# Kernel optimization log

Hardware: AMD Instinct MI355X
Metric: run time of the kernel (lower is better)

## Reference

```python
import jax, jax.numpy as jnp
import numpy as np


def _binomial_blur(k, C):
    a = np.array([1.0, 2.0, 1.0]) if k == 3 else np.ones(k)
    f = a[:, None] * a[None, :]
    f = f / f.sum()
    # HWIO depthwise kernel: (k, k, 1, C)
    return jnp.asarray(np.broadcast_to(f[:, :, None, None], (k, k, 1, C)).copy(), jnp.float32)


def setup_inputs() -> dict:
    key = jax.random.key(0)
    x = jax.random.normal(key, (32, 64, 64, 128), dtype=jnp.float32)
    blur_kernel = _binomial_blur(3, 128)  # fixed (non-learned) binomial low-pass filter
    return {"x": x, "blur_kernel": blur_kernel}


def reference(x, blur_kernel):
    B, T, F, C = x.shape
    # 1) 2x2 max pool, stride 1, SAME (pool_mode='max')
    p = jax.lax.reduce_window(x, -jnp.inf, jax.lax.max,
                              (1, 2, 2, 1), (1, 1, 1, 1), 'SAME')
    # 2) depthwise antialiasing blur, 3x3, SAME
    b = jax.lax.conv_general_dilated(
        p, blur_kernel, window_strides=(1, 1), padding='SAME',
        dimension_numbers=('NHWC', 'HWIO', 'NHWC'), feature_group_count=C)
    # 3) polyphase decomposition (stride 2). Order matches permute_polyphase:
    #    p0=(even,even), p1=(odd,even), p2=(even,odd), p3=(odd,odd)
    cands = jnp.stack([b[:, 0::2, 0::2], b[:, 1::2, 0::2],
                       b[:, 0::2, 1::2], b[:, 1::2, 1::2]], axis=1)  # [B,4,T/2,F/2,C]
    # 4) l2 criterion: pick candidate with max l2 norm per example
    norms = jnp.sqrt(jnp.sum(cands * cands, axis=(2, 3, 4)))  # [B,4]
    idx = jnp.argmax(norms, axis=1)  # [B]
    # 5) gather selected polyphase component
    out = jnp.take_along_axis(cands, idx[:, None, None, None, None], axis=1)[:, 0]
    return out  # [B, T/2, F/2, C]
```

## Files before the change

kernel.cpp:

```cpp
#include <hip/hip_runtime.h>
#include <hip/hip_bf16.h>
#include <float.h>


#define NEGF (-FLT_MAX)

__device__ __forceinline__ float4 f4max(float4 a, float4 b) {
    return make_float4(fmaxf(a.x, b.x), fmaxf(a.y, b.y),
                       fmaxf(a.z, b.z), fmaxf(a.w, b.w));
}
__device__ __forceinline__ float4 f4add(float4 a, float4 b) {
    return make_float4(a.x + b.x, a.y + b.y, a.z + b.z, a.w + b.w);
}
__device__ __forceinline__ float4 f4b3(float4 a, float4 b, float4 c) {
    return make_float4(fmaf(2.f, b.x, a.x + c.x), fmaf(2.f, b.y, a.y + c.y),
                       fmaf(2.f, b.z, a.z + c.z), fmaf(2.f, b.w, a.w + c.w));
}
__device__ __forceinline__ float4 Z4() { return make_float4(0.f, 0.f, 0.f, 0.f); }

__device__ __forceinline__ float bf2f(unsigned short h) {
    return __uint_as_float((unsigned)h << 16);
}
__device__ __forceinline__ ushort2 pk2(float a, float b) {
    __hip_bfloat162 h = __float22bfloat162_rn(make_float2(a, b));
    union { __hip_bfloat162 h2; ushort2 u2; } cv; cv.h2 = h;
    return cv.u2;
}
__device__ __forceinline__ ushort4 packbf(float4 v, float s) {
    ushort2 lo = pk2(v.x * s, v.y * s);
    ushort2 hi = pk2(v.z * s, v.w * s);
    ushort4 r; r.x = lo.x; r.y = lo.y; r.z = hi.x; r.w = hi.y;
    return r;
}

__device__ __forceinline__ void load_hm(const float4* __restrict__ xb, int r,
                                        const int voff[7], float4 hm[6]) {
    if (r < 0 || r > 63) {
#pragma unroll
        for (int j = 0; j < 6; ++j) hm[j] = make_float4(NEGF, NEGF, NEGF, NEGF);
        return;
    }
    const float4* row = xb + (size_t)r * (64 * 32);
    float4 xv[7];
#pragma unroll
    for (int j = 0; j < 7; ++j) xv[j] = row[voff[j]];
#pragma unroll
    for (int j = 0; j < 6; ++j) hm[j] = f4max(xv[j], xv[j + 1]);
}

__global__ __launch_bounds__(256, 2) void aps_norm_store_kernel(
        const float* __restrict__ xg, float4* __restrict__ partial4,
        ushort4* __restrict__ cand) {
    int blk = blockIdx.x;
    int h = blk & 7, ct = (blk >> 3) & 1, b = blk >> 4;
    int tid = threadIdx.x;
    int cg = tid & 31;
    int gc = ct * 8 + (tid >> 5);
    int C = gc * 4;
    int t0 = h * 8;

    const float4* xb = (const float4*)xg + (size_t)b * (64 * 64 * 32);

    int voff[7];
#pragma unroll
    for (int j = 0; j < 7; ++j) {
        int c = C - 1 + j;
        c = c < 0 ? 0 : (c > 63 ? 63 : c);
        voff[j] = c * 32 + cg;
    }
    bool zp0 = (gc == 0), zp5 = (gc == 15);

    float4 hmP[6];
    load_hm(xb, t0 - 1, voff, hmP);
    float4 xvA[7], xvB[7];
    {
        const float4* rowA = xb + (size_t)t0 * (64 * 32);
        const float4* rowB = xb + (size_t)(t0 + 1) * (64 * 32);
#pragma unroll
        for (int j = 0; j < 7; ++j) xvA[j] = rowA[voff[j]];
#pragma unroll
        for (int j = 0; j < 7; ++j) xvB[j] = rowB[voff[j]];
    }

    float4 uM1[4], uM2[4];
#pragma unroll
    for (int j = 0; j < 4; ++j) { uM1[j] = Z4(); uM2[j] = Z4(); }
    float aEE = 0.f, aEO = 0.f, aOE = 0.f, aOO = 0.f;

#pragma unroll
    for (int i = 0; i < 10; ++i) {
        int pr = t0 - 1 + i;
        int rN = pr + 3; rN = rN > 63 ? 63 : rN;
        const float4* rowN = xb + (size_t)rN * (64 * 32);
        float4 xvN[7];
#pragma unroll
        for (int j = 0; j < 7; ++j) xvN[j] = rowN[voff[j]];

        bool rv = (pr + 1) <= 63;
        float4 hmN[6];
#pragma unroll
        for (int j = 0; j < 6; ++j)
            hmN[j] = rv ? f4max(xvA[j], xvA[j + 1])
                        : make_float4(NEGF, NEGF, NEGF, NEGF);

        float4 p[6];
#pragma unroll
        for (int j = 0; j < 6; ++j) p[j] = f4max(hmP[j], hmN[j]);
        if (zp0) p[0] = Z4();
        if (zp5) p[5] = Z4();
        bool urow = (pr >= 0) & (pr <= 63);
        float4 u[4];
#pragma unroll
        for (int j = 0; j < 4; ++j)
            u[j] = urow ? f4b3(p[j], p[j + 1], p[j + 2]) : Z4();

        if (i >= 2) {
            float4 bb[4];
            float sE = 0.f, sO = 0.f;
#pragma unroll
            for (int j = 0; j < 4; ++j) {
                bb[j] = f4b3(uM2[j], uM1[j], u[j]);
                float d = bb[j].x * bb[j].x + bb[j].y * bb[j].y
                        + bb[j].z * bb[j].z + bb[j].w * bb[j].w;
                if (j & 1) sO += d; else sE += d;
            }
            sE *= (1.f / 256.f); sO *= (1.f / 256.f);
            if ((i & 1) == 0) { aEE += sE; aEO += sO; }
            else              { aOE += sE; aOO += sO; }

            int tp = i & 1;
            int tt = (t0 + i - 2) >> 1;
            size_t rowbase = (((size_t)b * 32 + tt) * 32) * 32 + cg;
            size_t f0 = rowbase + (size_t)(2 * gc) * 32;
            size_t f1 = rowbase + (size_t)(2 * gc + 1) * 32;
            size_t rT = (size_t)tp * 1048576;
            size_t rF = (size_t)(tp + 2) * 1048576;
            cand[rT + f0] = packbf(bb[0], 0.0625f);
            cand[rF + f0] = packbf(bb[1], 0.0625f);
            cand[rT + f1] = packbf(bb[2], 0.0625f);
            cand[rF + f1] = packbf(bb[3], 0.0625f);
        }

#pragma unroll
        for (int j = 0; j < 6; ++j) hmP[j] = hmN[j];
#pragma unroll
        for (int j = 0; j < 7; ++j) { xvA[j] = xvB[j]; xvB[j] = xvN[j]; }
#pragma unroll
        for (int j = 0; j < 4; ++j) { uM2[j] = uM1[j]; uM1[j] = u[j]; }
    }

    __shared__ float4 sm4[256];
    sm4[tid] = make_float4(aEE, aEO, aOE, aOO);
    __syncthreads();
    for (int s = 128; s >= 1; s >>= 1) {
        if (tid < s) sm4[tid] = f4add(sm4[tid], sm4[tid + s]);
        __syncthreads();
    }
    if (tid == 0) partial4[blk] = sm4[0];
}

__global__ __launch_bounds__(256) void aps_copy_kernel(
        const ushort4* __restrict__ cand, const float4* __restrict__ partial4,
        float4* __restrict__ outg) {
    __shared__ int ksm;
    int b = blockIdx.x >> 7;
    if (threadIdx.x == 0) {
        float4 tot = Z4();
        for (int j = 0; j < 16; ++j) tot = f4add(tot, partial4[b * 16 + j]);
        float n0 = tot.x, n1 = tot.z, n2 = tot.y, n3 = tot.w;
        int k = 0; float best = n0;
        if (n1 > best) { best = n1; k = 1; }
        if (n2 > best) { best = n2; k = 2; }
        if (n3 > best) { best = n3; k = 3; }
        ksm = k;
    }
    __syncthreads();
    int k = ksm;
    int gid = blockIdx.x * 256 + threadIdx.x;
    ushort4 v = cand[(size_t)k * 1048576 + gid];
    outg[gid] = make_float4(bf2f(v.x), bf2f(v.y), bf2f(v.z), bf2f(v.w));
}


__global__ __launch_bounds__(256, 2) void aps_norm_kernel(
        const float* __restrict__ xg, float4* __restrict__ partial4) {
    int blk = blockIdx.x;
    int h = blk & 7, ct = (blk >> 3) & 1, b = blk >> 4;
    int tid = threadIdx.x;
    int cg = tid & 31;
    int gc = ct * 8 + (tid >> 5);
    int C = gc * 4;
    int t0 = h * 8;

    const float4* xb = (const float4*)xg + (size_t)b * (64 * 64 * 32);

    int voff[7];
#pragma unroll
    for (int j = 0; j < 7; ++j) {
        int c = C - 1 + j;
        c = c < 0 ? 0 : (c > 63 ? 63 : c);
        voff[j] = c * 32 + cg;
    }
    bool zp0 = (gc == 0), zp5 = (gc == 15);

    float4 hmP[6];
    load_hm(xb, t0 - 1, voff, hmP);
    float4 uM1[4], uM2[4];
#pragma unroll
    for (int j = 0; j < 4; ++j) { uM1[j] = Z4(); uM2[j] = Z4(); }
    float aEE = 0.f, aEO = 0.f, aOE = 0.f, aOO = 0.f;

#pragma unroll
    for (int i = 0; i < 10; ++i) {
        int pr = t0 - 1 + i;
        float4 hmN[6];
        load_hm(xb, pr + 1, voff, hmN);
        float4 p[6];
#pragma unroll
        for (int j = 0; j < 6; ++j) p[j] = f4max(hmP[j], hmN[j]);
        if (zp0) p[0] = Z4();
        if (zp5) p[5] = Z4();
        bool urow = (pr >= 0) & (pr <= 63);
        float4 u[4];
#pragma unroll
        for (int j = 0; j < 4; ++j)
            u[j] = urow ? f4b3(p[j], p[j + 1], p[j + 2]) : Z4();
#pragma unroll
        for (int j = 0; j < 6; ++j) hmP[j] = hmN[j];
        if (i >= 2) {
            float sE = 0.f, sO = 0.f;
#pragma unroll
            for (int j = 0; j < 4; ++j) {
                float4 bb = f4b3(uM2[j], uM1[j], u[j]);
                float d = bb.x * bb.x + bb.y * bb.y + bb.z * bb.z + bb.w * bb.w;
                if (j & 1) sO += d; else sE += d;
            }
            sE *= (1.f / 256.f); sO *= (1.f / 256.f);
            if ((i & 1) == 0) { aEE += sE; aEO += sO; }
            else              { aOE += sE; aOO += sO; }
        }
#pragma unroll
        for (int j = 0; j < 4; ++j) { uM2[j] = uM1[j]; uM1[j] = u[j]; }
    }

    __shared__ float4 sm4[256];
    sm4[tid] = make_float4(aEE, aEO, aOE, aOO);
    __syncthreads();
    for (int s = 128; s >= 1; s >>= 1) {
        if (tid < s) sm4[tid] = f4add(sm4[tid], sm4[tid + s]);
        __syncthreads();
    }
    if (tid == 0) partial4[blk] = sm4[0];
}

__global__ __launch_bounds__(256, 2) void aps_gather_kernel(
        const float* __restrict__ xg, const float4* __restrict__ partial4,
        float* __restrict__ outg) {
    int blk = blockIdx.x;
    int h = blk & 7, ct = (blk >> 3) & 1, b = blk >> 4;
    int tid = threadIdx.x;
    int cg = tid & 31;
    int gc = ct * 8 + (tid >> 5);
    int C = gc * 4;

    float4 tot = Z4();
    for (int j = 0; j < 16; ++j) tot = f4add(tot, partial4[b * 16 + j]);
    float n0 = tot.x, n1 = tot.z, n2 = tot.y, n3 = tot.w;
    int k = 0; float best = n0;
    if (n1 > best) { best = n1; k = 1; }
    if (n2 > best) { best = n2; k = 2; }
    if (n3 > best) { best = n3; k = 3; }
    int tp = k & 1, fp = k >> 1;

    const float4* xb = (const float4*)xg + (size_t)b * (64 * 64 * 32);
    float4* ob = (float4*)outg + (size_t)b * (32 * 32 * 32);

    int voff[7];
#pragma unroll
    for (int j = 0; j < 7; ++j) {
        int c = C - 1 + j;
        c = c < 0 ? 0 : (c > 63 ? 63 : c);
        voff[j] = c * 32 + cg;
    }
    bool zp0 = (gc == 0), zp5 = (gc == 15);

    int sbase = h * 8 + tp;
    float4 hmP[6];
    load_hm(xb, sbase - 1, voff, hmP);
    float4 uM1[2], uM2[2];
#pragma unroll
    for (int j = 0; j < 2; ++j) { uM1[j] = Z4(); uM2[j] = Z4(); }

#pragma unroll
    for (int i = 0; i < 9; ++i) {
        int pr = sbase - 1 + i;
        float4 hmN[6];
        load_hm(xb, pr + 1, voff, hmN);
        float4 p[6];
#pragma unroll
        for (int j = 0; j < 6; ++j) p[j] = f4max(hmP[j], hmN[j]);
        if (zp0) p[0] = Z4();
        if (zp5) p[5] = Z4();
        bool urow = (pr >= 0) & (pr <= 63);
        float4 u[2];
        if (fp == 0) {
            u[0] = urow ? f4b3(p[0], p[1], p[2]) : Z4();
            u[1] = urow ? f4b3(p[2], p[3], p[4]) : Z4();
        } else {
            u[0] = urow ? f4b3(p[1], p[2], p[3]) : Z4();
            u[1] = urow ? f4b3(p[3], p[4], p[5]) : Z4();
        }
#pragma unroll
        for (int j = 0; j < 6; ++j) hmP[j] = hmN[j];
        if (i >= 2 && (i & 1) == 0) {
            int tt = 4 * h + (i >> 1) - 1;
#pragma unroll
            for (int jj = 0; jj < 2; ++jj) {
                float4 bb = f4b3(uM2[jj], uM1[jj], u[jj]);
                bb.x *= 0.0625f; bb.y *= 0.0625f; bb.z *= 0.0625f; bb.w *= 0.0625f;
                int ff = 2 * gc + jj;
                ob[((size_t)tt * 32 + ff) * 32 + cg] = bb;
            }
        }
#pragma unroll
        for (int j = 0; j < 2; ++j) { uM2[j] = uM1[j]; uM1[j] = u[j]; }
    }
}

extern "C" void kernel_launch(void* const* d_in, const int* in_sizes, int n_in,
                              void* d_out, int out_size, void* d_ws, size_t ws_size,
                              hipStream_t stream) {
    const float* x = (const float*)d_in[0];
    float4* partial4 = (float4*)d_ws;
    const size_t CAND_OFF = 8192;
    const size_t CAND_BYTES = (size_t)4 * 32 * 32 * 32 * 128 * 2;
    float* out = (float*)d_out;

    if (ws_size >= CAND_OFF + CAND_BYTES) {
        ushort4* cand = (ushort4*)((char*)d_ws + CAND_OFF);
        aps_norm_store_kernel<<<512, 256, 0, stream>>>(x, partial4, cand);
        aps_copy_kernel<<<4096, 256, 0, stream>>>(cand, partial4, (float4*)out);
    } else {
        aps_norm_kernel<<<512, 256, 0, stream>>>(x, partial4);
        aps_gather_kernel<<<512, 256, 0, stream>>>(x, partial4, out);
    }
}
```

Measured before the change: 31.72 us.

## Halve per-thread column tile in norm-store kernel, doubling grid and occupancy

New measurement: 43.47 us. 37.0% more time.

```diff
diff --git a/kernel.cpp b/kernel.cpp
--- a/kernel.cpp
+++ b/kernel.cpp
@@ -33,58 +33,53 @@
     return r;
 }
 
-__device__ __forceinline__ void load_hm(const float4* __restrict__ xb, int r,
-                                        const int voff[7], float4 hm[6]) {
-    if (r < 0 || r > 63) {
-#pragma unroll
-        for (int j = 0; j < 6; ++j) hm[j] = make_float4(NEGF, NEGF, NEGF, NEGF);
-        return;
-    }
-    const float4* row = xb + (size_t)r * (64 * 32);
-    float4 xv[7];
-#pragma unroll
-    for (int j = 0; j < 7; ++j) xv[j] = row[voff[j]];
-#pragma unroll
-    for (int j = 0; j < 6; ++j) hm[j] = f4max(xv[j], xv[j + 1]);
-}
-
-__global__ __launch_bounds__(256, 2) void aps_norm_store_kernel(
+__global__ __launch_bounds__(256, 4) void aps_norm_store_kernel(
         const float* __restrict__ xg, float4* __restrict__ partial4,
         ushort4* __restrict__ cand) {
     int blk = blockIdx.x;
-    int h = blk & 7, ct = (blk >> 3) & 1, b = blk >> 4;
+    int h = blk & 7, ct = (blk >> 3) & 3, b = blk >> 5;
     int tid = threadIdx.x;
     int cg = tid & 31;
-    int gc = ct * 8 + (tid >> 5);
-    int C = gc * 4;
+    int P = ct * 8 + (tid >> 5);
+    int C = P * 2;
     int t0 = h * 8;
 
     const float4* xb = (const float4*)xg + (size_t)b * (64 * 64 * 32);
 
-    int voff[7];
-#pragma unroll
-    for (int j = 0; j < 7; ++j) {
+    int voff[5];
+#pragma unroll
+    for (int j = 0; j < 5; ++j) {
         int c = C - 1 + j;
         c = c < 0 ? 0 : (c > 63 ? 63 : c);
         voff[j] = c * 32 + cg;
     }
-    bool zp0 = (gc == 0), zp5 = (gc == 15);
-
-    float4 hmP[6];
-    load_hm(xb, t0 - 1, voff, hmP);
-    float4 xvA[7], xvB[7];
+    bool zpL = (P == 0), zpR = (P == 31);
+
+    float4 hmP[4];
+    if (t0 - 1 < 0) {
+#pragma unroll
+        for (int j = 0; j < 4; ++j) hmP[j] = make_float4(NEGF, NEGF, NEGF, NEGF);
+    } else {
+        const float4* rowP = xb + (size_t)(t0 - 1) * (64 * 32);
+        float4 xv[5];
+#pragma unroll
+        for (int j = 0; j < 5; ++j) xv[j] = rowP[voff[j]];
+#pragma unroll
+        for (int j = 0; j < 4; ++j) hmP[j] = f4max(xv[j], xv[j + 1]);
+    }
+    float4 xvA[5], xvB[5];
     {
         const float4* rowA = xb + (size_t)t0 * (64 * 32);
         const float4* rowB = xb + (size_t)(t0 + 1) * (64 * 32);
 #pragma unroll
-        for (int j = 0; j < 7; ++j) xvA[j] = rowA[voff[j]];
-#pragma unroll
-        for (int j = 0; j < 7; ++j) xvB[j] = rowB[voff[j]];
-    }
-
-    float4 uM1[4], uM2[4];
-#pragma unroll
-    for (int j = 0; j < 4; ++j) { uM1[j] = Z4(); uM2[j] = Z4(); }
+        for (int j = 0; j < 5; ++j) xvA[j] = rowA[voff[j]];
+#pragma unroll
+        for (int j = 0; j < 5; ++j) xvB[j] = rowB[voff[j]];
+    }
+
+    float4 uM1[2], uM2[2];
+#pragma unroll
+    for (int j = 0; j < 2; ++j) { uM1[j] = Z4(); uM2[j] = Z4(); }
     float aEE = 0.f, aEO = 0.f, aOE = 0.f, aOO = 0.f;
 
 #pragma unroll
@@ -92,61 +87,49 @@
         int pr = t0 - 1 + i;
         int rN = pr + 3; rN = rN > 63 ? 63 : rN;
         const float4* rowN = xb + (size_t)rN * (64 * 32);
-        float4 xvN[7];
-#pragma unroll
-        for (int j = 0; j < 7; ++j) xvN[j] = rowN[voff[j]];
+        float4 xvN[5];
+#pragma unroll
+        for (int j = 0; j < 5; ++j) xvN[j] = rowN[voff[j]];
 
         bool rv = (pr + 1) <= 63;
-        float4 hmN[6];
-#pragma unroll
-        for (int j = 0; j < 6; ++j)
+        float4 hmN[4];
+#pragma unroll
+        for (int j = 0; j < 4; ++j)
             hmN[j] = rv ? f4max(xvA[j], xvA[j + 1])
                         : make_float4(NEGF, NEGF, NEGF, NEGF);
 
-        float4 p[6];
-#pragma unroll
-        for (int j = 0; j < 6; ++j) p[j] = f4max(hmP[j], hmN[j]);
-        if (zp0) p[0] = Z4();
-        if (zp5) p[5] = Z4();
+        float4 p[4];
+#pragma unroll
+        for (int j = 0; j < 4; ++j) p[j] = f4max(hmP[j], hmN[j]);
+        if (zpL) p[0] = Z4();
+        if (zpR) p[3] = Z4();
         bool urow = (pr >= 0) & (pr <= 63);
-        float4 u[4];
-#pragma unroll
-        for (int j = 0; j < 4; ++j)
-            u[j] = urow ? f4b3(p[j], p[j + 1], p[j + 2]) : Z4();
+        float4 u[2];
+        u[0] = urow ? f4b3(p[0], p[1], p[2]) : Z4();
+        u[1] = urow ? f4b3(p[1], p[2], p[3]) : Z4();
 
         if (i >= 2) {
-            float4 bb[4];
-            float sE = 0.f, sO = 0.f;
-#pragma unroll
-            for (int j = 0; j < 4; ++j) {
-                bb[j] = f4b3(uM2[j], uM1[j], u[j]);
-                float d = bb[j].x * bb[j].x + bb[j].y * bb[j].y
-                        + bb[j].z * bb[j].z + bb[j].w * bb[j].w;
-                if (j & 1) sO += d; else sE += d;
-            }
-            sE *= (1.f / 256.f); sO *= (1.f / 256.f);
-            if ((i & 1) == 0) { aEE += sE; aEO += sO; }
-            else              { aOE += sE; aOO += sO; }
+            float4 bb0 = f4b3(uM2[0], uM1[0], u[0]);
+            float4 bb1 = f4b3(uM2[1], uM1[1], u[1]);
+            float dE = bb0.x * bb0.x + bb0.y * bb0.y + bb0.z * bb0.z + bb0.w * bb0.w;
+            float dO = bb1.x * bb1.x + bb1.y * bb1.y + bb1.z * bb1.z + bb1.w * bb1.w;
+            dE *= (1.f / 256.f); dO *= (1.f / 256.f);
+            if ((i & 1) == 0) { aEE += dE; aEO += dO; }
+            else              { aOE += dE; aOO += dO; }
 
             int tp = i & 1;
             int tt = (t0 + i - 2) >> 1;
-            size_t rowbase = (((size_t)b * 32 + tt) * 32) * 32 + cg;
-            size_t f0 = rowbase + (size_t)(2 * gc) * 32;
-            size_t f1 = rowbase + (size_t)(2 * gc + 1) * 32;
-            size_t rT = (size_t)tp * 1048576;
-            size_t rF = (size_t)(tp + 2) * 1048576;
-            cand[rT + f0] = packbf(bb[0], 0.0625f);
-            cand[rF + f0] = packbf(bb[1], 0.0625f);
-            cand[rT + f1] = packbf(bb[2], 0.0625f);
-            cand[rF + f1] = packbf(bb[3], 0.0625f);
+            size_t foff = (((size_t)b * 32 + tt) * 32 + P) * 32 + cg;
+            cand[(size_t)tp * 1048576 + foff]       = packbf(bb0, 0.0625f);
+            cand[(size_t)(tp + 2) * 1048576 + foff] = packbf(bb1, 0.0625f);
         }
 
 #pragma unroll
-        for (int j = 0; j < 6; ++j) hmP[j] = hmN[j];
-#pragma unroll
-        for (int j = 0; j < 7; ++j) { xvA[j] = xvB[j]; xvB[j] = xvN[j]; }
-#pragma unroll
-        for (int j = 0; j < 4; ++j) { uM2[j] = uM1[j]; uM1[j] = u[j]; }
+        for (int j = 0; j < 4; ++j) hmP[j] = hmN[j];
+#pragma unroll
+        for (int j = 0; j < 5; ++j) { xvA[j] = xvB[j]; xvB[j] = xvN[j]; }
+#pragma unroll
+        for (int j = 0; j < 2; ++j) { uM2[j] = uM1[j]; uM1[j] = u[j]; }
     }
 
     __shared__ float4 sm4[256];
@@ -166,7 +149,7 @@
     int b = blockIdx.x >> 7;
     if (threadIdx.x == 0) {
         float4 tot = Z4();
-        for (int j = 0; j < 16; ++j) tot = f4add(tot, partial4[b * 16 + j]);
+        for (int j = 0; j < 32; ++j) tot = f4add(tot, partial4[b * 32 + j]);
         float n0 = tot.x, n1 = tot.z, n2 = tot.y, n3 = tot.w;
         int k = 0; float best = n0;
         if (n1 > best) { best = n1; k = 1; }
@@ -181,6 +164,21 @@
     outg[gid] = make_float4(bf2f(v.x), bf2f(v.y), bf2f(v.z), bf2f(v.w));
 }
 
+
+__device__ __forceinline__ void load_hm7(const float4* __restrict__ xb, int r,
+                                         const int voff[7], float4 hm[6]) {
+    if (r < 0 || r > 63) {
+#pragma unroll
+        for (int j = 0; j < 6; ++j) hm[j] = make_float4(NEGF, NEGF, NEGF, NEGF);
+        return;
+    }
+    const float4* row = xb + (size_t)r * (64 * 32);
+    float4 xv[7];
+#pragma unroll
+    for (int j = 0; j < 7; ++j) xv[j] = row[voff[j]];
+#pragma unroll
+    for (int j = 0; j < 6; ++j) hm[j] = f4max(xv[j], xv[j + 1]);
+}
 
 __global__ __launch_bounds__(256, 2) void aps_norm_kernel(
         const float* __restrict__ xg, float4* __restrict__ partial4) {
@@ -204,7 +202,7 @@
     bool zp0 = (gc == 0), zp5 = (gc == 15);
 
     float4 hmP[6];
-    load_hm(xb, t0 - 1, voff, hmP);
+    load_hm7(xb, t0 - 1, voff, hmP);
     float4 uM1[4], uM2[4];
 #pragma unroll
     for (int j = 0; j < 4; ++j) { uM1[j] = Z4(); uM2[j] = Z4(); }
@@ -214,7 +212,7 @@
     for (int i = 0; i < 10; ++i) {
         int pr = t0 - 1 + i;
         float4 hmN[6];
-        load_hm(xb, pr + 1, voff, hmN);
+        load_hm7(xb, pr + 1, voff, hmN);
         float4 p[6];
 #pragma unroll
         for (int j = 0; j < 6; ++j) p[j] = f4max(hmP[j], hmN[j]);
@@ -286,7 +284,7 @@
 
     int sbase = h * 8 + tp;
     float4 hmP[6];
-    load_hm(xb, sbase - 1, voff, hmP);
+    load_hm7(xb, sbase - 1, voff, hmP);
     float4 uM1[2], uM2[2];
 #pragma unroll
     for (int j = 0; j < 2; ++j) { uM1[j] = Z4(); uM2[j] = Z4(); }
@@ -295,7 +293,7 @@
     for (int i = 0; i < 9; ++i) {
         int pr = sbase - 1 + i;
         float4 hmN[6];
-        load_hm(xb, pr + 1, voff, hmN);
+        load_hm7(xb, pr + 1, voff, hmN);
         float4 p[6];
 #pragma unroll
         for (int j = 0; j < 6; ++j) p[j] = f4max(hmP[j], hmN[j]);
@@ -332,13 +330,13 @@
                               hipStream_t stream) {
     const float* x = (const float*)d_in[0];
     float4* partial4 = (float4*)d_ws;
-    const size_t CAND_OFF = 8192;
+    const size_t CAND_OFF = 16384;
     const size_t CAND_BYTES = (size_t)4 * 32 * 32 * 32 * 128 * 2;
     float* out = (float*)d_out;
 
     if (ws_size >= CAND_OFF + CAND_BYTES) {
         ushort4* cand = (ushort4*)((char*)d_ws + CAND_OFF);
-        aps_norm_store_kernel<<<512, 256, 0, stream>>>(x, partial4, cand);
+        aps_norm_store_kernel<<<1024, 256, 0, stream>>>(x, partial4, cand);
         aps_copy_kernel<<<4096, 256, 0, stream>>>(cand, partial4, (float4*)out);
     } else {
         aps_norm_kernel<<<512, 256, 0, stream>>>(x, partial4);
```
